# Optimization experiments

Hardware: AMD Instinct MI355X
Metric: run time of the kernel (lower is better)

The kernel has to match this reference:

```python
import jax, jax.numpy as jnp
import numpy as np

B, NP, FEAT, DEG, H = 16, 1024, 512, 16, 1024
E = B * NP * DEG
RATIO = 0.8


def setup_inputs() -> dict:
    key = jax.random.key(0)
    ks = jax.random.split(key, 16)
    x = jax.random.normal(ks[0], (B * NP, FEAT), jnp.float32)
    g = jnp.repeat(jnp.arange(B, dtype=jnp.int32), NP * DEG)
    src = jax.random.randint(ks[1], (E,), 0, NP, jnp.int32) + g * NP
    dst = jax.random.randint(ks[2], (E,), 0, NP, jnp.int32) + g * NP
    edge_index = jnp.stack([src, dst])
    batch = jnp.repeat(jnp.arange(B, dtype=jnp.int32), NP)
    sc = 0.02
    inp = dict(x=x, edge_index=edge_index, batch=batch)
    # SAGEConv params: out = lin_l(mean_agg) + lin_r(x); bias only on lin_l (PyG default)
    inp['W1l'] = sc * jax.random.normal(ks[3], (H, FEAT), jnp.float32)
    inp['b1'] = jnp.zeros((H,), jnp.float32)
    inp['W1r'] = sc * jax.random.normal(ks[4], (H, FEAT), jnp.float32)
    inp['p1'] = jax.random.normal(ks[5], (H,), jnp.float32)
    inp['W2l'] = sc * jax.random.normal(ks[6], (H, H), jnp.float32)
    inp['b2'] = jnp.zeros((H,), jnp.float32)
    inp['W2r'] = sc * jax.random.normal(ks[7], (H, H), jnp.float32)
    inp['p2'] = jax.random.normal(ks[8], (H,), jnp.float32)
    inp['W3l'] = sc * jax.random.normal(ks[9], (H, H), jnp.float32)
    inp['b3'] = jnp.zeros((H,), jnp.float32)
    inp['W3r'] = sc * jax.random.normal(ks[10], (H, H), jnp.float32)
    inp['p3'] = jax.random.normal(ks[11], (H,), jnp.float32)
    return inp


def _sage(x, src, dst, w, Wl, b, Wr, n_nodes):
    # mean aggregation over (masked) incoming edges, isolated nodes -> 0
    deg = jax.ops.segment_sum(w, dst, num_segments=n_nodes)
    agg = jax.ops.segment_sum(x[src] * w[:, None], dst, num_segments=n_nodes)
    mean = agg / jnp.maximum(deg, 1.0)[:, None]
    return mean @ Wl.T + b + x @ Wr.T


def _topk_pool(x, src, dst, mask, p, n_per):
    # PyG TopKPooling: score = tanh((x.w)/||w||); keep top ceil(ratio*n) per graph
    k = int(np.ceil(RATIO * n_per))
    s = jnp.tanh((x @ p) / jnp.linalg.norm(p))
    vals, idx = jax.lax.top_k(s.reshape(B, n_per), k)          # [B,k]
    old = (idx + (jnp.arange(B, dtype=idx.dtype) * n_per)[:, None]).reshape(-1)
    x_new = x[old] * vals.reshape(-1)[:, None]                  # gate kept nodes by score
    remap = jnp.full((B * n_per,), -1, jnp.int32).at[old].set(jnp.arange(B * k, dtype=jnp.int32))
    s2, d2 = remap[src], remap[dst]
    m2 = mask & (s2 >= 0) & (d2 >= 0)                           # drop edges losing an endpoint
    return x_new, jnp.where(m2, s2, 0), jnp.where(m2, d2, 0), m2, k


def _readout(x, n_per):
    xr = x.reshape(B, n_per, H)
    return jnp.concatenate([xr.max(axis=1), xr.mean(axis=1)], axis=1)  # [B, 2H]


def reference(x, edge_index, batch, W1l, b1, W1r, p1, W2l, b2, W2r, p2, W3l, b3, W3r, p3):
    src, dst = edge_index[0], edge_index[1]
    mask = jnp.ones((src.shape[0],), bool)
    n = NP
    h = jax.nn.relu(_sage(x, src, dst, mask.astype(x.dtype), W1l, b1, W1r, B * n))
    h, src, dst, mask, n = _topk_pool(h, src, dst, mask, p1, n)
    x1 = _readout(h, n)
    h = jax.nn.relu(_sage(h, src, dst, mask.astype(h.dtype), W2l, b2, W2r, B * n))
    h, src, dst, mask, n = _topk_pool(h, src, dst, mask, p2, n)
    x2 = _readout(h, n)
    h = jax.nn.relu(_sage(h, src, dst, mask.astype(h.dtype), W3l, b3, W3r, B * n))
    h, src, dst, mask, n = _topk_pool(h, src, dst, mask, p3, n)
    x3 = _readout(h, n)
    return x1 + x2 + x3
```

## Files before the change

kernel.cpp:

```cpp
#include <hip/hip_runtime.h>
#include <math.h>

#define B_    16
#define NP_   1024
#define FEAT_ 512
#define H_    1024
#define E_    262144
#define EPG_  16384
#define K1_   820
#define K2_   656
#define K3_   525
#define M1_   16384
#define M2_   13120
#define M3_   10496
#define MP1_  16384
#define MP2_  13312
#define MP3_  11264
#define SPROWS_ 16384

typedef unsigned short ushort_t;
typedef __bf16 bf16x8 __attribute__((ext_vector_type(8)));
typedef float f32x4 __attribute__((ext_vector_type(4)));

__device__ inline ushort_t f2bf(float f) {
    unsigned u = __float_as_uint(f);
    u += 0x7FFF + ((u >> 16) & 1);
    return (ushort_t)(u >> 16);
}
__device__ inline float bf2f(ushort_t h) {
    return __uint_as_float(((unsigned)h) << 16);
}
__device__ inline void split1(float v, ushort_t& hi, ushort_t& lo) {
    hi = f2bf(v);
    lo = f2bf(v - bf2f(hi));
}

__device__ inline void gll16(const void* g, void* l) {
    __builtin_amdgcn_global_load_lds((__attribute__((address_space(1))) void*)g,
                                     (__attribute__((address_space(3))) void*)l, 16, 0, 0);
}


__global__ __launch_bounds__(1024) void prep2_kernel(const int* __restrict__ ei,
                                                     int* __restrict__ counts,
                                                     int* __restrict__ offsets,
                                                     int* __restrict__ adj,
                                                     const float* __restrict__ p1,
                                                     const float* __restrict__ p2,
                                                     const float* __restrict__ p3,
                                                     float* __restrict__ pnout,
                                                     const float* __restrict__ W1l, const float* __restrict__ W1r,
                                                     const float* __restrict__ W2l, const float* __restrict__ W2r,
                                                     const float* __restrict__ W3l, const float* __restrict__ W3r,
                                                     ushort_t* __restrict__ Wb1, ushort_t* __restrict__ Wb2,
                                                     ushort_t* __restrict__ Wb3) {
    int t = threadIdx.x;
    if (blockIdx.x < 16) {
        __shared__ int cnt[1024];
        __shared__ int scanb[1024];
        int b = blockIdx.x;
        int e0 = b * EPG_;
        cnt[t] = 0;
        __syncthreads();
        for (int e = e0 + t; e < e0 + EPG_; e += 1024)
            atomicAdd(&cnt[ei[E_ + e] - b * NP_], 1);
        __syncthreads();
        int v = cnt[t];
        scanb[t] = v;
        __syncthreads();
        for (int off = 1; off < 1024; off <<= 1) {
            int tv = (t >= off) ? scanb[t - off] : 0;
            __syncthreads();
            scanb[t] += tv;
            __syncthreads();
        }
        int excl = scanb[t] - v;
        counts[b * NP_ + t] = v;
        offsets[b * NP_ + t] = e0 + excl;
        cnt[t] = excl;
        __syncthreads();
        for (int e = e0 + t; e < e0 + EPG_; e += 1024) {
            int s = ei[e];
            int dloc = ei[E_ + e] - b * NP_;
            int pos = atomicAdd(&cnt[dloc], 1);
            adj[e0 + pos] = s;
        }
        return;
    }
    if (blockIdx.x < 19) {
        const float* p = blockIdx.x == 16 ? p1 : (blockIdx.x == 17 ? p2 : p3);
        __shared__ float red[1024];
        float a = p[t];
        red[t] = a * a;
        __syncthreads();
        for (int s = 512; s > 0; s >>= 1) {
            if (t < s) red[t] += red[t + s];
            __syncthreads();
        }
        if (t == 0) pnout[blockIdx.x - 16] = sqrtf(red[0]);
        return;
    }
    int idx = (blockIdx.x - 19) * 1024 + t;
    if (idx >= 524288 + 1048576 + 1048576) return;
    const float *Wl, *Wr; ushort_t* Wbig; int K;
    if (idx < 524288) { Wl = W1l; Wr = W1r; Wbig = Wb1; K = 512; }
    else if (idx < 524288 + 1048576) { idx -= 524288; Wl = W2l; Wr = W2r; Wbig = Wb2; K = 1024; }
    else { idx -= 524288 + 1048576; Wl = W3l; Wr = W3r; Wbig = Wb3; K = 1024; }
    int n = idx / K;
    int k = idx - n * K;
    ushort_t* row = Wbig + (size_t)n * (4 * K);
    float a = Wl[idx];
    ushort_t ah = f2bf(a);
    row[k] = ah;
    row[K + k] = f2bf(a - bf2f(ah));
    float b = Wr[idx];
    ushort_t bh = f2bf(b);
    row[2 * K + k] = bh;
    row[3 * K + k] = f2bf(b - bf2f(bh));
}


__global__ __launch_bounds__(128) void agg1_k512(const float* __restrict__ x,
                                                 const int* __restrict__ adj,
                                                 const int* __restrict__ offsets,
                                                 const int* __restrict__ counts,
                                                 ushort_t* __restrict__ Abig) {
    int gid = blockIdx.x;
    int xcd = gid & 7;
    int u = gid >> 3;
    int half = u & 1;
    int pi = u >> 1;
    int gsel = (pi >= 512) ? 1 : 0;
    int g = xcd + (gsel << 3);
    int node = g * 1024 + (pi - (gsel << 9)) * 2 + (threadIdx.x >> 6);
    int c = threadIdx.x & 63;
    int col4 = half * 64 + c;
    int start = offsets[node], cnt = counts[node];
    float d = fmaxf((float)cnt, 1.0f);
    const float4* xb = (const float4*)x;
    float ax = 0.f, ay = 0.f, az = 0.f, aw = 0.f;
    int j = 0;
    for (; j + 8 <= cnt; j += 8) {
        int si[8];
#pragma unroll
        for (int q = 0; q < 8; ++q) si[q] = adj[start + j + q];
        float4 vv[8];
#pragma unroll
        for (int q = 0; q < 8; ++q) vv[q] = xb[(size_t)si[q] * 128 + col4];
#pragma unroll
        for (int q = 0; q < 8; ++q) {
            ax += vv[q].x; ay += vv[q].y; az += vv[q].z; aw += vv[q].w;
        }
    }
    for (; j + 4 <= cnt; j += 4) {
        int s0 = adj[start + j + 0], s1 = adj[start + j + 1];
        int s2 = adj[start + j + 2], s3 = adj[start + j + 3];
        float4 v0 = xb[(size_t)s0 * 128 + col4];
        float4 v1 = xb[(size_t)s1 * 128 + col4];
        float4 v2 = xb[(size_t)s2 * 128 + col4];
        float4 v3 = xb[(size_t)s3 * 128 + col4];
        ax += (v0.x + v1.x) + (v2.x + v3.x);
        ay += (v0.y + v1.y) + (v2.y + v3.y);
        az += (v0.z + v1.z) + (v2.z + v3.z);
        aw += (v0.w + v1.w) + (v2.w + v3.w);
    }
    for (; j < cnt; ++j) {
        float4 v = xb[(size_t)adj[start + j] * 128 + col4];
        ax += v.x; ay += v.y; az += v.z; aw += v.w;
    }
    float inv = 1.0f / d;
    float4 cv = xb[(size_t)node * 128 + col4];
    ushort_t* row = Abig + (size_t)node * 2048;
    int f = col4 * 4;
    ushort4 mh, ml, ch, cl;
    split1(ax * inv, mh.x, ml.x); split1(ay * inv, mh.y, ml.y);
    split1(az * inv, mh.z, ml.z); split1(aw * inv, mh.w, ml.w);
    split1(cv.x, ch.x, cl.x); split1(cv.y, ch.y, cl.y);
    split1(cv.z, ch.z, cl.z); split1(cv.w, ch.w, cl.w);
    *(ushort4*)&row[f]        = mh;
    *(ushort4*)&row[512 + f]  = ml;
    *(ushort4*)&row[1024 + f] = ch;
    *(ushort4*)&row[1536 + f] = cl;
}

template<int LAYER>
__global__ __launch_bounds__(128) void agg23_k1024(const float* __restrict__ h,
                                                   const int* __restrict__ adj,
                                                   const int* __restrict__ offsets,
                                                   const int* __restrict__ counts,
                                                   const int* __restrict__ old_idx,
                                                   const float* __restrict__ vals,
                                                   ushort_t* __restrict__ Abig,
                                                   int n_per, int M, int npad) {
    int gid = blockIdx.x;
    if (gid >= 32 * n_per) {
        int r = gid - 32 * n_per;
        if (r < npad) {
            uint4* row = (uint4*)(Abig + (size_t)(M + r) * 4096);
#pragma unroll
            for (int q = 0; q < 4; ++q) row[threadIdx.x + q * 128] = (uint4){0, 0, 0, 0};
        }
        return;
    }
    int xcd = gid & 7;
    int u = gid >> 3;
    int half = u & 1;
    int nl = u >> 1;
    int gsel = (nl >= n_per) ? 1 : 0;
    int g = xcd + (gsel << 3);
    int node = g * n_per + nl - gsel * n_per;
    int c = threadIdx.x;
    int col4 = half * 128 + c;
    int start = offsets[node], cnt = counts[node];
    float d = fmaxf((float)cnt, 1.0f);
    const float4* hb = (const float4*)h;
    float ax = 0.f, ay = 0.f, az = 0.f, aw = 0.f;
    int j = 0;
    for (; j + 8 <= cnt; j += 8) {
        int si[8];
#pragma unroll
        for (int q = 0; q < 8; ++q) si[q] = adj[start + j + q];
        int oi[8]; float wi[8];
#pragma unroll
        for (int q = 0; q < 8; ++q) { oi[q] = old_idx[si[q]]; wi[q] = vals[si[q]]; }
        float4 vv[8];
#pragma unroll
        for (int q = 0; q < 8; ++q) vv[q] = hb[(size_t)oi[q] * 256 + col4];
#pragma unroll
        for (int q = 0; q < 8; ++q) {
            ax += wi[q] * vv[q].x; ay += wi[q] * vv[q].y;
            az += wi[q] * vv[q].z; aw += wi[q] * vv[q].w;
        }
    }
    for (; j + 4 <= cnt; j += 4) {
        int s0 = adj[start + j + 0], s1 = adj[start + j + 1];
        int s2 = adj[start + j + 2], s3 = adj[start + j + 3];
        int o0 = old_idx[s0], o1 = old_idx[s1], o2 = old_idx[s2], o3 = old_idx[s3];
        float w0 = vals[s0], w1 = vals[s1], w2 = vals[s2], w3 = vals[s3];
        float4 v0 = hb[(size_t)o0 * 256 + col4];
        float4 v1 = hb[(size_t)o1 * 256 + col4];
        float4 v2 = hb[(size_t)o2 * 256 + col4];
        float4 v3 = hb[(size_t)o3 * 256 + col4];
        ax += (w0 * v0.x + w1 * v1.x) + (w2 * v2.x + w3 * v3.x);
        ay += (w0 * v0.y + w1 * v1.y) + (w2 * v2.y + w3 * v3.y);
        az += (w0 * v0.z + w1 * v1.z) + (w2 * v2.z + w3 * v3.z);
        aw += (w0 * v0.w + w1 * v1.w) + (w2 * v2.w + w3 * v3.w);
    }
    for (; j < cnt; ++j) {
        int s = adj[start + j];
        int o = old_idx[s];
        float w = vals[s];
        float4 v = hb[(size_t)o * 256 + col4];
        ax += w * v.x; ay += w * v.y; az += w * v.z; aw += w * v.w;
    }
    float inv = 1.0f / d;
    int on = old_idx[node];
    float vn = vals[node];
    float4 cv = hb[(size_t)on * 256 + col4];
    cv.x *= vn; cv.y *= vn; cv.z *= vn; cv.w *= vn;
    ushort_t* row = Abig + (size_t)node * 4096;
    int f = col4 * 4;
    ushort4 mh, ml, ch, cl;
    split1(ax * inv, mh.x, ml.x); split1(ay * inv, mh.y, ml.y);
    split1(az * inv, mh.z, ml.z); split1(aw * inv, mh.w, ml.w);
    split1(cv.x, ch.x, cl.x); split1(cv.y, ch.y, cl.y);
    split1(cv.z, ch.z, cl.z); split1(cv.w, ch.w, cl.w);
    *(ushort4*)&row[f]        = mh;
    *(ushort4*)&row[1024 + f] = ml;
    *(ushort4*)&row[2048 + f] = ch;
    *(ushort4*)&row[3072 + f] = cl;
}


template<int LAYER>
__global__ __launch_bounds__(256) void gemm_mfma(const ushort_t* __restrict__ Ab,
                                                 const ushort_t* __restrict__ Wb,
                                                 const float* __restrict__ bias,
                                                 float* __restrict__ C,
                                                 float* __restrict__ sp,
                                                 const float* __restrict__ pvec,
                                                 int K, int npanels) {
    __shared__ ushort_t lA0[4096];
    __shared__ ushort_t lA1[4096];
    __shared__ ushort_t lB0[4096];
    __shared__ ushort_t lB1[4096];
    const int LD = 4 * K;
    int tid = threadIdx.x;
    int lane = tid & 63;
    int w = tid >> 6;
    int wr = (w >> 1) * 64, wc = (w & 1) * 64;

    int gid = blockIdx.x;
    int xcd = gid & 7;
    int idx = gid >> 3;
    int panel = xcd * (npanels >> 3) + (idx >> 3);
    int cb = idx & 7;
    int m0 = panel * 128, n0 = cb * 128;

    int srow = tid >> 2;
    int gq = (tid & 3) ^ ((tid >> 2) & 3) ^ ((tid >> 4) & 3);
    const ushort_t* Ag = Ab + (size_t)(m0 + srow) * LD + gq * 8;
    const ushort_t* Bg = Wb + (size_t)(n0 + srow) * LD + gq * 8;
    ushort_t* lA0p = &lA0[tid * 8];
    ushort_t* lA1p = &lA1[tid * 8];
    ushort_t* lB0p = &lB0[tid * 8];
    ushort_t* lB1p = &lB1[tid * 8];
    const size_t rstep = (size_t)64 * LD;

    int qsw = (lane >> 4) ^ (lane & 3) ^ ((lane >> 2) & 3);
    int aidx = (wr + (lane & 15)) * 32 + qsw * 8;
    int bidx = (wc + (lane & 15)) * 32 + qsw * 8;

    f32x4 acc[4][4];
#pragma unroll
    for (int i = 0; i < 4; ++i)
#pragma unroll
        for (int j = 0; j < 4; ++j) acc[i][j] = (f32x4){0.f, 0.f, 0.f, 0.f};

    for (int ss = 0; ss < 2; ++ss) {
        const ushort_t* Ah = Ag + ss * 2 * K;
        const ushort_t* Bh = Bg + ss * 2 * K;
        for (int kk = 0; kk < K; kk += 32) {
            __syncthreads();
            gll16(Ah + kk, lA0p);
            gll16(Ah + kk + rstep, lA0p + 2048);
            gll16(Ah + K + kk, lA1p);
            gll16(Ah + K + kk + rstep, lA1p + 2048);
            gll16(Bh + kk, lB0p);
            gll16(Bh + kk + rstep, lB0p + 2048);
            gll16(Bh + K + kk, lB1p);
            gll16(Bh + K + kk + rstep, lB1p + 2048);
            __syncthreads();
            bf16x8 a0[4], a1[4], b0[4], b1[4];
#pragma unroll
            for (int i = 0; i < 4; ++i) a0[i] = *(const bf16x8*)&lA0[aidx + i * 512];
#pragma unroll
            for (int j = 0; j < 4; ++j) b0[j] = *(const bf16x8*)&lB0[bidx + j * 512];
#pragma unroll
            for (int i = 0; i < 4; ++i)
#pragma unroll
                for (int j = 0; j < 4; ++j)
                    acc[i][j] = __builtin_amdgcn_mfma_f32_16x16x32_bf16(a0[i], b0[j], acc[i][j], 0, 0, 0);
#pragma unroll
            for (int i = 0; i < 4; ++i) a1[i] = *(const bf16x8*)&lA1[aidx + i * 512];
#pragma unroll
            for (int i = 0; i < 4; ++i)
#pragma unroll
                for (int j = 0; j < 4; ++j)
                    acc[i][j] = __builtin_amdgcn_mfma_f32_16x16x32_bf16(a1[i], b0[j], acc[i][j], 0, 0, 0);
#pragma unroll
            for (int j = 0; j < 4; ++j) b1[j] = *(const bf16x8*)&lB1[bidx + j * 512];
#pragma unroll
            for (int i = 0; i < 4; ++i)
#pragma unroll
                for (int j = 0; j < 4; ++j)
                    acc[i][j] = __builtin_amdgcn_mfma_f32_16x16x32_bf16(a0[i], b1[j], acc[i][j], 0, 0, 0);
        }
    }

    float bj[4], pj[4];
#pragma unroll
    for (int j = 0; j < 4; ++j) {
        int col = n0 + wc + j * 16 + (lane & 15);
        bj[j] = bias[col];
        pj[j] = pvec[col];
    }
    int slot = cb * 2 + (wc >> 6);
#pragma unroll
    for (int i = 0; i < 4; ++i) {
        int row0 = m0 + wr + i * 16 + (lane >> 4) * 4;
        float sacc[4] = {0.f, 0.f, 0.f, 0.f};
#pragma unroll
        for (int j = 0; j < 4; ++j) {
            int col = n0 + wc + j * 16 + (lane & 15);
#pragma unroll
            for (int r = 0; r < 4; ++r) {
                float v = acc[i][j][r] + bj[j];
                v = v > 0.f ? v : 0.f;
                C[(size_t)(row0 + r) * 1024 + col] = v;
                sacc[r] += v * pj[j];
            }
        }
#pragma unroll
        for (int r = 0; r < 4; ++r) {
            float sv_ = sacc[r];
            sv_ += __shfl_xor(sv_, 1);
            sv_ += __shfl_xor(sv_, 2);
            sv_ += __shfl_xor(sv_, 4);
            sv_ += __shfl_xor(sv_, 8);
            if ((lane & 15) == 0) sp[slot * SPROWS_ + row0 + r] = sv_;
        }
    }
}


template<int FIRST>
__global__ __launch_bounds__(1024) void tail_kernel(const float* __restrict__ sp,
                                                    const float* __restrict__ pn,
                                                    const float* __restrict__ h,
                                                    float* __restrict__ out,
                                                    int n, int k,
                                                    int* __restrict__ old_idx, float* __restrict__ vals,
                                                    const int* __restrict__ ei,
                                                    int* __restrict__ esrc, int* __restrict__ edst,
                                                    int* __restrict__ emask,
                                                    int* __restrict__ counts, int* __restrict__ offsets,
                                                    int* __restrict__ adj, int do_edges) {
    __shared__ float sv[1024];
    __shared__ int   rmap[1024];
    __shared__ int   oi_s[1024];
    __shared__ float vv_s[1024];
    __shared__ float4 rmx[32][32];
    __shared__ float4 rsm[32][32];
    int b = blockIdx.x / 9, role = blockIdx.x % 9;
    int t = threadIdx.x;
    if (role == 8 && !do_edges) return;

    float mine = -INFINITY;
    if (t < n) {
        int base = b * n + t;
        float s0 = 0.f;
#pragma unroll
        for (int c = 0; c < 16; ++c) s0 += sp[c * SPROWS_ + base];
        mine = s0;
    }
    sv[t] = mine;
    __syncthreads();
    int rank = 0;
#pragma unroll 4
    for (int j = 0; j < 1024; ++j) {
        float o = sv[j];
        rank += (o > mine) || (o == mine && j < t);
    }
    bool kept = (t < n) && (rank < k);
    rmap[t] = kept ? rank : -1;
    if (kept) {
        float tv = tanhf(mine / pn[0]);
        oi_s[rank] = b * n + t;
        vv_s[rank] = tv;
        if (role == 8) {
            old_idx[b * k + rank] = b * n + t;
            vals[b * k + rank] = tv;
        }
    }
    __syncthreads();

    if (role < 8) {
        int c32 = t & 31, g = t >> 5;
        int col4 = role * 32 + c32;
        const float4* hb = (const float4*)h;
        float4 mx = {-INFINITY, -INFINITY, -INFINITY, -INFINITY};
        float4 sm = {0.f, 0.f, 0.f, 0.f};
        for (int i = g; i < k; i += 32) {
            int o = oi_s[i];
            float wgt = vv_s[i];
            float4 v = hb[(size_t)o * 256 + col4];
            v.x *= wgt; v.y *= wgt; v.z *= wgt; v.w *= wgt;
            mx.x = fmaxf(mx.x, v.x); mx.y = fmaxf(mx.y, v.y);
            mx.z = fmaxf(mx.z, v.z); mx.w = fmaxf(mx.w, v.w);
            sm.x += v.x; sm.y += v.y; sm.z += v.z; sm.w += v.w;
        }
        rmx[g][c32] = mx; rsm[g][c32] = sm;
        __syncthreads();
        for (int s = 16; s > 0; s >>= 1) {
            if (g < s) {
                float4 om = rmx[g + s][c32], os = rsm[g + s][c32];
                float4 m = rmx[g][c32], ss2 = rsm[g][c32];
                m.x = fmaxf(m.x, om.x); m.y = fmaxf(m.y, om.y);
                m.z = fmaxf(m.z, om.z); m.w = fmaxf(m.w, om.w);
                ss2.x += os.x; ss2.y += os.y; ss2.z += os.z; ss2.w += os.w;
                rmx[g][c32] = m; rsm[g][c32] = ss2;
            }
            __syncthreads();
        }
        if (g == 0) {
            float4 m = rmx[0][c32], ss2 = rsm[0][c32];
            float invk = 1.0f / (float)k;
            float* o0 = out + (size_t)b * 2048 + col4 * 4;
            float* o1 = o0 + 1024;
            if (FIRST) {
                o0[0] = m.x; o0[1] = m.y; o0[2] = m.z; o0[3] = m.w;
                o1[0] = ss2.x * invk; o1[1] = ss2.y * invk;
                o1[2] = ss2.z * invk; o1[3] = ss2.w * invk;
            } else {
                o0[0] += m.x; o0[1] += m.y; o0[2] += m.z; o0[3] += m.w;
                o1[0] += ss2.x * invk; o1[1] += ss2.y * invk;
                o1[2] += ss2.z * invk; o1[3] += ss2.w * invk;
            }
        }
        return;
    }

    __shared__ int cnt_s[1024];
    cnt_s[t] = 0;
    __syncthreads();
    int e0 = b * EPG_;
    for (int e = e0 + t; e < e0 + EPG_; e += 1024) {
        int ms = FIRST ? 1 : emask[e];
        if (ms) {
            int s = FIRST ? ei[e] : esrc[e];
            int dd = FIRST ? ei[E_ + e] : edst[e];
            int ns = rmap[s - b * n];
            int nd = rmap[dd - b * n];
            if (ns >= 0 && nd >= 0) atomicAdd(&cnt_s[nd], 1);
        }
    }
    __syncthreads();
    int v = (t < k) ? cnt_s[t] : 0;
    oi_s[t] = v;
    __syncthreads();
    for (int off = 1; off < 1024; off <<= 1) {
        int tv = (t >= off) ? oi_s[t - off] : 0;
        __syncthreads();
        oi_s[t] += tv;
        __syncthreads();
    }
    int excl = oi_s[t] - v;
    if (t < k) {
        counts[b * k + t] = v;
        offsets[b * k + t] = e0 + excl;
        cnt_s[t] = excl;
    }
    __syncthreads();
    for (int e = e0 + t; e < e0 + EPG_; e += 1024) {
        int ms = FIRST ? 1 : emask[e];
        if (ms) {
            int s = FIRST ? ei[e] : esrc[e];
            int dd = FIRST ? ei[E_ + e] : edst[e];
            int ns = rmap[s - b * n];
            int nd = rmap[dd - b * n];
            if (ns >= 0 && nd >= 0) {
                int gs = b * k + ns;
                esrc[e] = gs;
                edst[e] = b * k + nd;
                if (FIRST) emask[e] = 1;
                int pos = atomicAdd(&cnt_s[nd], 1);
                adj[e0 + pos] = gs;
            } else {
                emask[e] = 0;
            }
        } else if (FIRST) {
            emask[e] = 0;
        }
    }
}


extern "C" void kernel_launch(void* const* d_in, const int* in_sizes, int n_in,
                              void* d_out, int out_size, void* d_ws, size_t ws_size,
                              hipStream_t stream) {
    const float* x   = (const float*)d_in[0];
    const int*   ei  = (const int*)d_in[1];
    const float* W1l = (const float*)d_in[3];
    const float* b1  = (const float*)d_in[4];
    const float* W1r = (const float*)d_in[5];
    const float* p1  = (const float*)d_in[6];
    const float* W2l = (const float*)d_in[7];
    const float* b2  = (const float*)d_in[8];
    const float* W2r = (const float*)d_in[9];
    const float* p2  = (const float*)d_in[10];
    const float* W3l = (const float*)d_in[11];
    const float* b3  = (const float*)d_in[12];
    const float* W3r = (const float*)d_in[13];
    const float* p3  = (const float*)d_in[14];
    float* out = (float*)d_out;

    char* ws = (char*)d_ws;
    size_t off = 0;
    float* bufOut = (float*)(ws + off); off += (size_t)MP1_ * 1024 * 4;
    ushort_t* Abig = (ushort_t*)(ws + off); off += (size_t)MP2_ * 4096 * 2;
    ushort_t* Wb1 = (ushort_t*)(ws + off); off += (size_t)1024 * 2048 * 2;
    ushort_t* Wb2 = (ushort_t*)(ws + off); off += (size_t)1024 * 4096 * 2;
    ushort_t* Wb3 = (ushort_t*)(ws + off); off += (size_t)1024 * 4096 * 2;
    float* sp = (float*)(ws + off); off += (size_t)16 * SPROWS_ * 4;
    char* misc = ws + off;
    int*   counts = (int*)(misc + 0 * 65536);
    int*   offsets= (int*)(misc + 1 * 65536);
    int*   old_idx= (int*)(misc + 2 * 65536);
    float* vals   = (float*)(misc + 3 * 65536);
    float* pnormv = (float*)(misc + 4 * 65536);
    int*   adj    = (int*)(misc + 5 * 65536);
    int*   esrc   = (int*)(misc + 5 * 65536 + 1 * 1048576);
    int*   edst   = (int*)(misc + 5 * 65536 + 2 * 1048576);
    int*   emask  = (int*)(misc + 5 * 65536 + 3 * 1048576);

    prep2_kernel<<<19 + (524288 + 2 * 1048576) / 1024, 1024, 0, stream>>>(
        ei, counts, offsets, adj, p1, p2, p3, pnormv,
        W1l, W1r, W2l, W2r, W3l, W3r, Wb1, Wb2, Wb3);

    agg1_k512<<<16384, 128, 0, stream>>>(x, adj, offsets, counts, Abig);
    gemm_mfma<1><<<(MP1_ / 128) * 8, 256, 0, stream>>>(Abig, Wb1, b1, bufOut, sp, p1, 512, MP1_ / 128);
    tail_kernel<1><<<B_ * 9, 1024, 0, stream>>>(sp, pnormv + 0, bufOut, out, NP_, K1_,
                                                old_idx, vals, ei, esrc, edst, emask,
                                                counts, offsets, adj, 1);

    agg23_k1024<2><<<32 * K1_ + (MP2_ - M2_), 128, 0, stream>>>(
        bufOut, adj, offsets, counts, old_idx, vals, Abig, K1_, M2_, MP2_ - M2_);
    gemm_mfma<2><<<(MP2_ / 128) * 8, 256, 0, stream>>>(Abig, Wb2, b2, bufOut, sp, p2, 1024, MP2_ / 128);
    tail_kernel<0><<<B_ * 9, 1024, 0, stream>>>(sp, pnormv + 1, bufOut, out, K1_, K2_,
                                                old_idx, vals, ei, esrc, edst, emask,
                                                counts, offsets, adj, 1);

    agg23_k1024<3><<<32 * K2_ + (MP3_ - M3_), 128, 0, stream>>>(
        bufOut, adj, offsets, counts, old_idx, vals, Abig, K2_, M3_, MP3_ - M3_);
    gemm_mfma<3><<<(MP3_ / 128) * 8, 256, 0, stream>>>(Abig, Wb3, b3, bufOut, sp, p3, 1024, MP3_ / 128);
    tail_kernel<0><<<B_ * 9, 1024, 0, stream>>>(sp, pnormv + 2, bufOut, out, K2_, K3_,
                                                old_idx, vals, ei, esrc, edst, emask,
                                                counts, offsets, adj, 0);
}
```

Measured before the change: 860.9 us.

## Rewrite split-bf16 GEMM as 256x256-tile, double-buffered, interleaved load/MFMA pipeline

Replaces the 128x128 single-buffered GEMM (two syncthreads per k-step) with a 256x256 tile, 512-thread kernel. It double-buffers LDS and issues the next chunk's global-to-LDS loads interleaved with MFMA groups, using explicit vmcnt waits, raw barriers and s_setprio. This raises arithmetic intensity per byte loaded and hides load latency behind compute. In exchange it uses 128KB of LDS and a larger accumulator set, which limits occupancy. The tile count also drops, which may leave CUs idle: the 13312-row layer 2 gives 208 tiles and the 11264-row layer 3 gives 176.

```diff
diff --git a/kernel.cpp b/kernel.cpp
--- a/kernel.cpp
+++ b/kernel.cpp
@@ -272,107 +272,153 @@
 }
 
 
-template<int LAYER>
-__global__ __launch_bounds__(256) void gemm_mfma(const ushort_t* __restrict__ Ab,
-                                                 const ushort_t* __restrict__ Wb,
-                                                 const float* __restrict__ bias,
-                                                 float* __restrict__ C,
-                                                 float* __restrict__ sp,
-                                                 const float* __restrict__ pvec,
-                                                 int K, int npanels) {
-    __shared__ ushort_t lA0[4096];
-    __shared__ ushort_t lA1[4096];
-    __shared__ ushort_t lB0[4096];
-    __shared__ ushort_t lB1[4096];
-    const int LD = 4 * K;
+#define STR_(x) #x
+#define VMW2_(n) asm volatile("s_waitcnt vmcnt(" STR_(n) ")" ::: "memory")
+#define VMW(n) VMW2_(n)
+#define BARM() do { __builtin_amdgcn_s_barrier(); asm volatile("" ::: "memory"); } while (0)
+
+#define STG(Lw_, pl_, src_, c_) {                                                   \
+    const ushort_t* s_ = (src_) + (c_);                                             \
+    gll16(s_, (Lw_) + (pl_) * 8192);                                                \
+    gll16(s_ + rstep, (Lw_) + (pl_) * 8192 + 4096);                                 \
+}
+
+#define MFQ(I0, Aarr, A0, Barr)                                                     \
+    _Pragma("unroll")                                                               \
+    for (int ii = 0; ii < 4; ++ii) {                                                \
+        _Pragma("unroll")                                                           \
+        for (int jj = 0; jj < 4; ++jj)                                              \
+            acc[(I0) + ii][jj] = __builtin_amdgcn_mfma_f32_16x16x32_bf16(           \
+                Aarr[(A0) + ii], Barr[jj], acc[(I0) + ii][jj], 0, 0, 0);            \
+    }
+
+#define CHUNK(t_, b_, stg_, vb_, v1_, v3_) do {                                     \
+    int cn_ = ((t_) + 1 < NC2) ? ((t_) + 1) * 32 : 2 * KK + ((t_) + 1 - NC2) * 32;  \
+    const ushort_t* Lr = L + (b_) * 32768;                                          \
+    ushort_t* Lw = L + (1 - (b_)) * 32768 + tid * 8;                                \
+    VMW(vb_);                                                                       \
+    BARM();                                                                         \
+    bf16x8 ah[8], al[8], bh[4], bl[4];                                              \
+    _Pragma("unroll") for (int q = 0; q < 4; ++q)                                   \
+        ah[q] = *(const bf16x8*)&Lr[aoff + q * 512];                                \
+    _Pragma("unroll") for (int q = 0; q < 4; ++q)                                   \
+        bh[q] = *(const bf16x8*)&Lr[16384 + boff + q * 512];                        \
+                           \
+    _Pragma("unroll") for (int q = 0; q < 4; ++q)                                   \
+        ah[4 + q] = *(const bf16x8*)&Lr[aoff + (4 + q) * 512];                      \
+    if (stg_) { STG(Lw, 0, Ag, cn_); }                                              \
+    BARM();                                                                         \
+    __builtin_amdgcn_s_setprio(1);                                                  \
+    MFQ(0, ah, 0, bh);                                                              \
+    __builtin_amdgcn_s_setprio(0);                                                  \
+    VMW(v1_);                                                                       \
+    BARM();                                                                         \
+                           \
+    _Pragma("unroll") for (int q = 0; q < 4; ++q)                                   \
+        al[q] = *(const bf16x8*)&Lr[8192 + aoff + q * 512];                         \
+    if (stg_) { STG(Lw, 2, Bg, cn_); }                                              \
+    BARM();                                                                         \
+    __builtin_amdgcn_s_setprio(1);                                                  \
+    MFQ(4, ah, 4, bh);                                                              \
+    __builtin_amdgcn_s_setprio(0);                                                  \
+    BARM();                                                                         \
+                           \
+    _Pragma("unroll") for (int q = 0; q < 4; ++q)                                   \
+        al[4 + q] = *(const bf16x8*)&Lr[8192 + aoff + (4 + q) * 512];               \
+    if (stg_) { STG(Lw, 1, Ag + KK, cn_); }                                         \
+    BARM();                                                                         \
+    __builtin_amdgcn_s_setprio(1);                                                  \
+    MFQ(0, al, 0, bh);                                                              \
+    __builtin_amdgcn_s_setprio(0);                                                  \
+    VMW(v3_);                                                                       \
+    BARM();                                                                         \
+                           \
+    _Pragma("unroll") for (int q = 0; q < 4; ++q)                                   \
+        bl[q] = *(const bf16x8*)&Lr[24576 + boff + q * 512];                        \
+    if (stg_) { STG(Lw, 3, Bg + KK, cn_); }                                         \
+    BARM();                                                                         \
+    __builtin_amdgcn_s_setprio(1);                                                  \
+    MFQ(4, al, 4, bh);                                                              \
+    __builtin_amdgcn_s_setprio(0);                                                  \
+    BARM();                                                                         \
+                                   \
+    __builtin_amdgcn_s_setprio(1);                                                  \
+    MFQ(0, ah, 0, bl);                                                              \
+    MFQ(4, ah, 4, bl);                                                              \
+    __builtin_amdgcn_s_setprio(0);                                                  \
+} while (0)
+
+template<int KK>
+__global__ __launch_bounds__(512, 2) void gemm256(const ushort_t* __restrict__ Ab,
+                                                  const ushort_t* __restrict__ Wb,
+                                                  const float* __restrict__ bias,
+                                                  float* __restrict__ C,
+                                                  float* __restrict__ sp,
+                                                  const float* __restrict__ pvec,
+                                                  int npanels) {
+    constexpr int LD  = 4 * KK;
+    constexpr int NC  = KK / 16;
+    constexpr int NC2 = KK / 32;
+    __shared__ ushort_t L[65536];
+
     int tid = threadIdx.x;
     int lane = tid & 63;
     int w = tid >> 6;
-    int wr = (w >> 1) * 64, wc = (w & 1) * 64;
-
-    int gid = blockIdx.x;
-    int xcd = gid & 7;
-    int idx = gid >> 3;
-    int panel = xcd * (npanels >> 3) + (idx >> 3);
-    int cb = idx & 7;
-    int m0 = panel * 128, n0 = cb * 128;
+    int wm = w >> 2, wn = w & 3;
+
+    int nb = npanels * 4;
+    int per = nb >> 3;
+    int bp = (blockIdx.x & 7) * per + (blockIdx.x >> 3);
+    int panel = bp >> 2, cb = bp & 3;
+    int m0 = panel * 256, n0 = cb * 256;
 
     int srow = tid >> 2;
-    int gq = (tid & 3) ^ ((tid >> 2) & 3) ^ ((tid >> 4) & 3);
+    int gq = (tid & 3) ^ (srow & 3) ^ ((srow >> 2) & 3);
     const ushort_t* Ag = Ab + (size_t)(m0 + srow) * LD + gq * 8;
     const ushort_t* Bg = Wb + (size_t)(n0 + srow) * LD + gq * 8;
-    ushort_t* lA0p = &lA0[tid * 8];
-    ushort_t* lA1p = &lA1[tid * 8];
-    ushort_t* lB0p = &lB0[tid * 8];
-    ushort_t* lB1p = &lB1[tid * 8];
-    const size_t rstep = (size_t)64 * LD;
+    const size_t rstep = (size_t)128 * LD;
 
     int qsw = (lane >> 4) ^ (lane & 3) ^ ((lane >> 2) & 3);
-    int aidx = (wr + (lane & 15)) * 32 + qsw * 8;
-    int bidx = (wc + (lane & 15)) * 32 + qsw * 8;
-
-    f32x4 acc[4][4];
-#pragma unroll
-    for (int i = 0; i < 4; ++i)
+    int aoff = (wm * 128 + (lane & 15)) * 32 + qsw * 8;
+    int boff = (wn * 64 + (lane & 15)) * 32 + qsw * 8;
+
+    f32x4 acc[8][4];
+#pragma unroll
+    for (int i = 0; i < 8; ++i)
 #pragma unroll
         for (int j = 0; j < 4; ++j) acc[i][j] = (f32x4){0.f, 0.f, 0.f, 0.f};
 
-    for (int ss = 0; ss < 2; ++ss) {
-        const ushort_t* Ah = Ag + ss * 2 * K;
-        const ushort_t* Bh = Bg + ss * 2 * K;
-        for (int kk = 0; kk < K; kk += 32) {
-            __syncthreads();
-            gll16(Ah + kk, lA0p);
-            gll16(Ah + kk + rstep, lA0p + 2048);
-            gll16(Ah + K + kk, lA1p);
-            gll16(Ah + K + kk + rstep, lA1p + 2048);
-            gll16(Bh + kk, lB0p);
-            gll16(Bh + kk + rstep, lB0p + 2048);
-            gll16(Bh + K + kk, lB1p);
-            gll16(Bh + K + kk + rstep, lB1p + 2048);
-            __syncthreads();
-            bf16x8 a0[4], a1[4], b0[4], b1[4];
-#pragma unroll
-            for (int i = 0; i < 4; ++i) a0[i] = *(const bf16x8*)&lA0[aidx + i * 512];
-#pragma unroll
-            for (int j = 0; j < 4; ++j) b0[j] = *(const bf16x8*)&lB0[bidx + j * 512];
-#pragma unroll
-            for (int i = 0; i < 4; ++i)
-#pragma unroll
-                for (int j = 0; j < 4; ++j)
-                    acc[i][j] = __builtin_amdgcn_mfma_f32_16x16x32_bf16(a0[i], b0[j], acc[i][j], 0, 0, 0);
-#pragma unroll
-            for (int i = 0; i < 4; ++i) a1[i] = *(const bf16x8*)&lA1[aidx + i * 512];
-#pragma unroll
-            for (int i = 0; i < 4; ++i)
-#pragma unroll
-                for (int j = 0; j < 4; ++j)
-                    acc[i][j] = __builtin_amdgcn_mfma_f32_16x16x32_bf16(a1[i], b0[j], acc[i][j], 0, 0, 0);
-#pragma unroll
-            for (int j = 0; j < 4; ++j) b1[j] = *(const bf16x8*)&lB1[bidx + j * 512];
-#pragma unroll
-            for (int i = 0; i < 4; ++i)
-#pragma unroll
-                for (int j = 0; j < 4; ++j)
-                    acc[i][j] = __builtin_amdgcn_mfma_f32_16x16x32_bf16(a0[i], b1[j], acc[i][j], 0, 0, 0);
-        }
-    }
+    {
+        ushort_t* Lw0 = L + tid * 8;
+        STG(Lw0, 0, Ag, 0);
+        STG(Lw0, 2, Bg, 0);
+        STG(Lw0, 1, Ag + KK, 0);
+        STG(Lw0, 3, Bg + KK, 0);
+    }
+
+#pragma unroll 1
+    for (int t = 0; t < NC - 2; t += 2) {
+        CHUNK(t,     0, 1, 4, 4, 6);
+        CHUNK(t + 1, 1, 1, 4, 4, 6);
+    }
+    CHUNK(NC - 2, 0, 1, 4, 4, 6);
+    CHUNK(NC - 1, 1, 0, 4, 2, 0);
 
     float bj[4], pj[4];
 #pragma unroll
     for (int j = 0; j < 4; ++j) {
-        int col = n0 + wc + j * 16 + (lane & 15);
+        int col = n0 + wn * 64 + j * 16 + (lane & 15);
         bj[j] = bias[col];
         pj[j] = pvec[col];
     }
-    int slot = cb * 2 + (wc >> 6);
-#pragma unroll
-    for (int i = 0; i < 4; ++i) {
-        int row0 = m0 + wr + i * 16 + (lane >> 4) * 4;
+    int slot = cb * 4 + wn;
+#pragma unroll
+    for (int i = 0; i < 8; ++i) {
+        int row0 = m0 + wm * 128 + i * 16 + (lane >> 4) * 4;
         float sacc[4] = {0.f, 0.f, 0.f, 0.f};
 #pragma unroll
         for (int j = 0; j < 4; ++j) {
-            int col = n0 + wc + j * 16 + (lane & 15);
+            int col = n0 + wn * 64 + j * 16 + (lane & 15);
 #pragma unroll
             for (int r = 0; r < 4; ++r) {
                 float v = acc[i][j][r] + bj[j];
@@ -589,21 +635,21 @@
         W1l, W1r, W2l, W2r, W3l, W3r, Wb1, Wb2, Wb3);
 
     agg1_k512<<<16384, 128, 0, stream>>>(x, adj, offsets, counts, Abig);
-    gemm_mfma<1><<<(MP1_ / 128) * 8, 256, 0, stream>>>(Abig, Wb1, b1, bufOut, sp, p1, 512, MP1_ / 128);
+    gemm256<512><<<(MP1_ / 256) * 4, 512, 0, stream>>>(Abig, Wb1, b1, bufOut, sp, p1, MP1_ / 256);
     tail_kernel<1><<<B_ * 9, 1024, 0, stream>>>(sp, pnormv + 0, bufOut, out, NP_, K1_,
                                                 old_idx, vals, ei, esrc, edst, emask,
                                                 counts, offsets, adj, 1);
 
     agg23_k1024<2><<<32 * K1_ + (MP2_ - M2_), 128, 0, stream>>>(
         bufOut, adj, offsets, counts, old_idx, vals, Abig, K1_, M2_, MP2_ - M2_);
-    gemm_mfma<2><<<(MP2_ / 128) * 8, 256, 0, stream>>>(Abig, Wb2, b2, bufOut, sp, p2, 1024, MP2_ / 128);
+    gemm256<1024><<<(MP2_ / 256) * 4, 512, 0, stream>>>(Abig, Wb2, b2, bufOut, sp, p2, MP2_ / 256);
     tail_kernel<0><<<B_ * 9, 1024, 0, stream>>>(sp, pnormv + 1, bufOut, out, K1_, K2_,
                                                 old_idx, vals, ei, esrc, edst, emask,
                                                 counts, offsets, adj, 1);
 
     agg23_k1024<3><<<32 * K2_ + (MP3_ - M3_), 128, 0, stream>>>(
         bufOut, adj, offsets, counts, old_idx, vals, Abig, K2_, M3_, MP3_ - M3_);
-    gemm_mfma<3><<<(MP3_ / 128) * 8, 256, 0, stream>>>(Abig, Wb3, b3, bufOut, sp, p3, 1024, MP3_ / 128);
+    gemm256<1024><<<(MP3_ / 256) * 4, 512, 0, stream>>>(Abig, Wb3, b3, bufOut, sp, p3, MP3_ / 256);
     tail_kernel<0><<<B_ * 9, 1024, 0, stream>>>(sp, pnormv + 2, bufOut, out, K2_, K3_,
                                                 old_idx, vals, ei, esrc, edst, emask,
                                                 counts, offsets, adj, 0);
```

Result: faster. 773.4 us (-10.2%).
